# Kernel tuning notes

Hardware: AMD Instinct MI355X
Metric: run time of the kernel (lower is better)

## Reference

```python
import jax, jax.numpy as jnp
import numpy as np

N = 131072   # total nodes (4096 molecules x ~32 atoms)
E = 524288   # directed edges (avg degree 4)
G = 4096     # number of graphs
D_IN, D_H, D_OUT = 128, 512, 256
BN_EPS = 1e-5


def setup_inputs() -> dict:
    key = jax.random.key(0)
    ks = jax.random.split(key, 24)
    def rn(i, shape, s=0.05):
        return jax.random.normal(ks[i], shape, jnp.float32) * s
    inp = {
        "x": jax.random.normal(ks[0], (N, D_IN), jnp.float32),
        "edge_index": jax.random.randint(ks[1], (2, E), 0, N),
        "batch": jnp.sort(jax.random.randint(ks[2], (N,), 0, G)),
        # GCN layer weights (stored [in, out]) and biases
        "W1": rn(3, (D_IN, D_H)), "b1": jnp.zeros((D_H,), jnp.float32),
        "W2": rn(4, (D_H, D_H)),  "b2": jnp.zeros((D_H,), jnp.float32),
        "W3": rn(5, (D_H, D_OUT)), "b3": jnp.zeros((D_OUT,), jnp.float32),
        # BatchNorm (eval mode): gamma, beta, running_mean, running_var
        "g1": jnp.ones((D_H,), jnp.float32),  "be1": jnp.zeros((D_H,), jnp.float32),
        "m1": rn(6, (D_H,)),  "v1": jax.random.uniform(ks[7], (D_H,), jnp.float32) + 0.5,
        "g2": jnp.ones((D_H,), jnp.float32),  "be2": jnp.zeros((D_H,), jnp.float32),
        "m2": rn(8, (D_H,)),  "v2": jax.random.uniform(ks[9], (D_H,), jnp.float32) + 0.5,
        "g3": jnp.ones((D_OUT,), jnp.float32), "be3": jnp.zeros((D_OUT,), jnp.float32),
        "m3": rn(10, (D_OUT,)), "v3": jax.random.uniform(ks[11], (D_OUT,), jnp.float32) + 0.5,
        # MLP head
        "Wf1": rn(12, (D_OUT, D_OUT)), "bf1": jnp.zeros((D_OUT,), jnp.float32),
        "Wf2": rn(13, (D_OUT, D_OUT)), "bf2": jnp.zeros((D_OUT,), jnp.float32),
    }
    return inp


def reference(x, edge_index, batch, W1, b1, W2, b2, W3, b3,
              g1, be1, m1, v1, g2, be2, m2, v2, g3, be3, m3, v3,
              Wf1, bf1, Wf2, bf2):
    loop = jnp.arange(N)
    src = jnp.concatenate([edge_index[0], loop])  # add self-loops (PyG GCNConv default)
    dst = jnp.concatenate([edge_index[1], loop])
    deg = jax.ops.segment_sum(jnp.ones((E + N,), x.dtype), dst, num_segments=N)
    dinv = jnp.where(deg > 0, jax.lax.rsqrt(deg), 0.0)
    norm = dinv[src] * dinv[dst]                  # D^{-1/2} A_hat D^{-1/2}

    def gcn(h, W, b):
        h = h @ W                                 # dense GEMM [N, d_out]
        msg = h[src] * norm[:, None]              # gather + scale
        return jax.ops.segment_sum(msg, dst, num_segments=N) + b  # scatter-add

    def bn(h, g, be, m, v):                       # eval-mode BatchNorm1d
        return g * (h - m) * jax.lax.rsqrt(v + BN_EPS) + be

    h = bn(jax.nn.relu(gcn(x, W1, b1)), g1, be1, m1, v1)
    h = bn(jax.nn.relu(gcn(h, W2, b2)), g2, be2, m2, v2)
    h = bn(jax.nn.relu(gcn(h, W3, b3)), g3, be3, m3, v3)

    sums = jax.ops.segment_sum(h, batch, num_segments=G)          # global_mean_pool
    cnt = jax.ops.segment_sum(jnp.ones((N,), h.dtype), batch, num_segments=G)
    pooled = sums / jnp.maximum(cnt, 1.0)[:, None]

    return jax.nn.relu(pooled @ Wf1 + bf1) @ Wf2 + bf2
```

## Files before the change

### kernel.cpp

```cpp
#include <hip/hip_runtime.h>

static constexpr int NN = 131072;
static constexpr int NE = 524288;
static constexpr int NG = 4096;

typedef __attribute__((ext_vector_type(8))) short short8;
typedef __attribute__((ext_vector_type(4))) float f32x4;
typedef __attribute__((ext_vector_type(2))) float f32x2;

__device__ __forceinline__ float bfbits2f(unsigned b) {
    return __uint_as_float(b << 16);
}
__device__ __forceinline__ unsigned short f2bfbits(float f) {
    unsigned u = __float_as_uint(f);
    u += 0x7fffu + ((u >> 16) & 1u);
    return (unsigned short)(u >> 16);
}
__device__ __forceinline__ unsigned pack2(float a, float b) {
    return (unsigned)f2bfbits(a) | ((unsigned)f2bfbits(b) << 16);
}

__device__ __forceinline__ int geti(const void* p, size_t i, int w64) {
    return w64 ? (int)((const long long*)p)[i] : ((const int*)p)[i];
}
__device__ __forceinline__ int e64_of(const void* eidx) {
    const int* e = (const int*)eidx;
    return (e[1] == 0 && e[2001] == 0 && e[40001] == 0 && e[2 * NE - 1] == 0) ? 1 : 0;
}
__device__ __forceinline__ int b64_of(const void* batch) {
    return (((const int*)batch)[NN - 1] == 0) ? 1 : 0;
}

#if __has_builtin(__builtin_amdgcn_cvt_pk_f32_fp8) && __has_builtin(__builtin_amdgcn_cvt_pk_fp8_f32)
#define FP8_CVT_HW 1
#else
#define FP8_CVT_HW 0
#endif

__device__ __forceinline__ float e4m32f(unsigned b) {
    unsigned e = (b >> 3) & 0xFu, m = b & 7u;
    float v = e ? __uint_as_float(((e + 120u) << 23) | (m << 20))
                : (float)m * 0.001953125f;
    return (b & 0x80u) ? -v : v;
}
__device__ __forceinline__ unsigned f2e4m3(float f) {
    unsigned u = __float_as_uint(f);
    unsigned s = (u >> 24) & 0x80u;
    unsigned mag = u & 0x7fffffffu;
    if (mag >= 0x43e00000u) return s | 0x7eu;
    if (mag < 0x3c800000u) {
        int q = (int)(__uint_as_float(mag) * 512.0f + 0.5f);
        return s | (unsigned)q;
    }
    unsigned r = mag + 0x0007ffffu + ((mag >> 20) & 1u);
    if (r >= 0x43e00000u) return s | 0x7eu;
    return s | (((r >> 23) - 120u) << 3) | ((r >> 20) & 7u);
}

template<bool HI>
__device__ __forceinline__ unsigned dec_pair(unsigned w) {
#if FP8_CVT_HW
    f32x2 p = __builtin_amdgcn_cvt_pk_f32_fp8((int)w, HI);
    return __builtin_amdgcn_perm(__float_as_uint(p.y), __float_as_uint(p.x), 0x07060302u);
#else
    unsigned b0 = HI ? ((w >> 16) & 255u) : (w & 255u);
    unsigned b1 = HI ? (w >> 24) : ((w >> 8) & 255u);
    return pack2(e4m32f(b0), e4m32f(b1));
#endif
}

__device__ __forceinline__ short8 dec8(uint2 u) {
    union { uint4 q; short8 s; } r;
    r.q.x = dec_pair<false>(u.x);
    r.q.y = dec_pair<true>(u.x);
    r.q.z = dec_pair<false>(u.y);
    r.q.w = dec_pair<true>(u.y);
    return r.s;
}

__device__ __forceinline__ void dec4f(unsigned w, float* v) {
#if FP8_CVT_HW
    f32x2 a = __builtin_amdgcn_cvt_pk_f32_fp8((int)w, false);
    f32x2 b = __builtin_amdgcn_cvt_pk_f32_fp8((int)w, true);
    v[0] = a.x; v[1] = a.y; v[2] = b.x; v[3] = b.y;
#else
#pragma unroll
    for (int i = 0; i < 4; ++i) v[i] = e4m32f((w >> (8 * i)) & 0xffu);
#endif
}

__device__ __forceinline__ unsigned enc4(float a, float b, float c, float d) {
#if FP8_CVT_HW
    int r = __builtin_amdgcn_cvt_pk_fp8_f32(a, b, 0, false);
    r = __builtin_amdgcn_cvt_pk_fp8_f32(c, d, r, true);
    return (unsigned)r;
#else
    return f2e4m3(a) | (f2e4m3(b) << 8) | (f2e4m3(c) << 16) | (f2e4m3(d) << 24);
#endif
}
__device__ __forceinline__ unsigned enc1(float a) {
#if FP8_CVT_HW
    return (unsigned)__builtin_amdgcn_cvt_pk_fp8_f32(a, a, 0, false) & 0xffu;
#else
    return f2e4m3(a);
#endif
}

__device__ __forceinline__ void bf8f(uint4 u, float* v) {
    v[0] = bfbits2f(u.x & 0xffffu); v[1] = bfbits2f(u.x >> 16);
    v[2] = bfbits2f(u.y & 0xffffu); v[3] = bfbits2f(u.y >> 16);
    v[4] = bfbits2f(u.z & 0xffffu); v[5] = bfbits2f(u.z >> 16);
    v[6] = bfbits2f(u.w & 0xffffu); v[7] = bfbits2f(u.w >> 16);
}

__device__ __forceinline__ void gld16(const void* g, void* l, int lane) {
#if __has_builtin(__builtin_amdgcn_global_load_lds)
    __builtin_amdgcn_global_load_lds((const __attribute__((address_space(1))) unsigned int*)g,
                                     (__attribute__((address_space(3))) unsigned int*)l, 16, 0, 0);
#else
    *(uint4*)((char*)l + lane * 16) = *(const uint4*)g;
#endif
}

__global__ __launch_bounds__(256) void k_prep(
    const float* __restrict__ W1, const float* __restrict__ W2, const float* __restrict__ W3,
    const float* __restrict__ Wf1, const float* __restrict__ Wf2,
    unsigned short* __restrict__ Wt1, unsigned short* __restrict__ Wt2,
    unsigned short* __restrict__ Wt3, unsigned short* __restrict__ Wtf1,
    unsigned short* __restrict__ Wtf2,
    const float* __restrict__ g1, const float* __restrict__ be1,
    const float* __restrict__ m1, const float* __restrict__ v1,
    const float* __restrict__ g2, const float* __restrict__ be2,
    const float* __restrict__ m2, const float* __restrict__ v2,
    const float* __restrict__ g3, const float* __restrict__ be3,
    const float* __restrict__ m3, const float* __restrict__ v3,
    float* __restrict__ sbuf, int* __restrict__ cnt2,
    const void* __restrict__ batch, int* __restrict__ gstart)
{
    const int id = blockIdx.x, tid = threadIdx.x;
    if (id < 1024) {
        int idx = id * 256 + tid; int k = idx >> 9, n = idx & 511;
        Wt2[n * 512 + k] = f2bfbits(W2[idx]);
    } else if (id < 1536) {
        int idx = (id - 1024) * 256 + tid; int k = idx >> 8, n = idx & 255;
        Wt3[n * 512 + k] = f2bfbits(W3[idx]);
    } else if (id < 1792) {
        int idx = (id - 1536) * 256 + tid; int k = idx >> 9, n = idx & 511;
        Wt1[n * 128 + k] = f2bfbits(W1[idx]);
    } else if (id < 2048) {
        int idx = (id - 1792) * 256 + tid; int k = idx >> 8, n = idx & 255;
        Wtf1[n * 256 + k] = f2bfbits(Wf1[idx]);
    } else if (id < 2304) {
        int idx = (id - 2048) * 256 + tid; int k = idx >> 8, n = idx & 255;
        Wtf2[n * 256 + k] = f2bfbits(Wf2[idx]);
    } else if (id < 3328) {
        cnt2[(id - 2304) * 256 + tid] = 0;
    } else if (id < 3333) {
        int i = (id - 3328) * 256 + tid;
        if (i < 512) {
            float inv = rsqrtf(v1[i] + 1e-5f); float sc = g1[i] * inv;
            sbuf[i] = sc; sbuf[512 + i] = be1[i] - m1[i] * sc;
        } else if (i < 1024) {
            int j = i - 512;
            float inv = rsqrtf(v2[j] + 1e-5f); float sc = g2[j] * inv;
            sbuf[1024 + j] = sc; sbuf[1536 + j] = be2[j] - m2[j] * sc;
        } else if (i < 1280) {
            int j = i - 1024;
            float inv = rsqrtf(v3[j] + 1e-5f); float sc = g3[j] * inv;
            sbuf[2048 + j] = sc; sbuf[2304 + j] = be3[j] - m3[j] * sc;
        }
    } else {
        int i = (id - 3333) * 256 + tid;
        if (i >= NN) return;
        int b64 = b64_of(batch);
        int b = geti(batch, (size_t)i, b64);
        if (i == 0) {
            for (int g = 0; g <= b; ++g) gstart[g] = 0;
        } else {
            int pb = geti(batch, (size_t)i - 1, b64);
            for (int g = pb + 1; g <= b; ++g) gstart[g] = i;
        }
        if (i == NN - 1) {
            for (int g = b + 1; g <= NG; ++g) gstart[g] = NN;
        }
    }
}

__global__ void k_deg_count(const void* __restrict__ eidx, int* __restrict__ cnt) {
    int i = blockIdx.x * 256 + threadIdx.x;
    if (i >= NE) return;
    int d = geti(eidx, (size_t)NE + i, e64_of(eidx));
    atomicAdd(&cnt[d], 1);
}

__global__ __launch_bounds__(256) void k_scan_a(const int* __restrict__ cnt, int* __restrict__ bsum) {
    __shared__ int red[256];
    const int t = threadIdx.x;
    int2 u = *(const int2*)(cnt + blockIdx.x * 512 + t * 2);
    red[t] = u.x + u.y;
    __syncthreads();
    for (int off = 128; off > 0; off >>= 1) {
        if (t < off) red[t] += red[t + off];
        __syncthreads();
    }
    if (t == 0) bsum[blockIdx.x] = red[0];
}

__global__ __launch_bounds__(256) void k_scan_b(const int* __restrict__ bsum, int* __restrict__ boff,
                                                int* __restrict__ rowptr) {
    __shared__ int part[256];
    const int t = threadIdx.x;
    int v = bsum[t];
    part[t] = v;
    __syncthreads();
    for (int off = 1; off < 256; off <<= 1) {
        int w = (t >= off) ? part[t - off] : 0;
        __syncthreads();
        part[t] += w;
        __syncthreads();
    }
    boff[t] = part[t] - v;
    if (t == 255) rowptr[NN] = part[255];
}

__global__ __launch_bounds__(256) void k_scan_c(const int* __restrict__ cnt, const int* __restrict__ boff,
                                                int* __restrict__ rowptr, float* __restrict__ dinv) {
    __shared__ int part[256];
    const int t = threadIdx.x;
    const int base = blockIdx.x * 512 + t * 2;
    int2 u = *(const int2*)(cnt + base);
    int s = u.x + u.y;
    part[t] = s;
    __syncthreads();
    for (int off = 1; off < 256; off <<= 1) {
        int w = (t >= off) ? part[t - off] : 0;
        __syncthreads();
        part[t] += w;
        __syncthreads();
    }
    int ex = boff[blockIdx.x] + part[t] - s;
    int2 o; o.x = ex; o.y = ex + u.x;
    *(int2*)(rowptr + base) = o;
    float2 dv;
    dv.x = rsqrtf((float)(u.x + 1));
    dv.y = rsqrtf((float)(u.y + 1));
    *(float2*)(dinv + base) = dv;
}

__global__ void k_fill(const void* __restrict__ eidx,
                       const int* __restrict__ rowptr, int* __restrict__ fillp,
                       int* __restrict__ col) {
    int i = blockIdx.x * 256 + threadIdx.x;
    if (i >= NE) return;
    int e64 = e64_of(eidx);
    int s = geti(eidx, (size_t)i, e64);
    int d = geti(eidx, (size_t)NE + i, e64);
    int p = rowptr[d] + atomicAdd(&fillp[d], 1);
    col[p] = s;
}

template<int D, int MODE>
__device__ __forceinline__ void load_row_hw(const void* h, int sn, int c0, float* v) {
    if constexpr (MODE == 2) {
        float4 u = *(const float4*)((const float*)h + (size_t)sn * D + c0);
        v[0] = u.x; v[1] = u.y; v[2] = u.z; v[3] = u.w;
    } else {
        uint4 u = *(const uint4*)((const unsigned char*)h + (size_t)sn * D + c0);
        dec4f(u.x, v); dec4f(u.y, v + 4); dec4f(u.z, v + 8); dec4f(u.w, v + 12);
    }
}

template<int D, int EPL, bool FP8>
__device__ __forceinline__ void store_row_hw(void* out, int n, int c0, const float* v) {
    if constexpr (FP8) {
        uint4 u;
        u.x = enc4(v[0], v[1], v[2], v[3]);
        u.y = enc4(v[4], v[5], v[6], v[7]);
        u.z = enc4(v[8], v[9], v[10], v[11]);
        u.w = enc4(v[12], v[13], v[14], v[15]);
        *(uint4*)((unsigned char*)out + (size_t)n * D + c0) = u;
    } else {
        uint2 u; u.x = pack2(v[0], v[1]); u.y = pack2(v[2], v[3]);
        *(uint2*)((unsigned short*)out + (size_t)n * D + c0) = u;
    }
}

template<int D, int IN_MODE, bool OUT_FP8>
__global__ __launch_bounds__(256) void k_agg_hw(
    const void* __restrict__ h,
    const int* __restrict__ rowptr, const int* __restrict__ col,
    const float* __restrict__ dinv,
    void* __restrict__ out)
{
    constexpr int EPL = (IN_MODE == 1) ? 16 : 4;
    const int n = (blockIdx.x * 256 + threadIdx.x) >> 5;
    const int lane = threadIdx.x & 31;
    const int c0 = lane * EPL;
    float dn = dinv[n];
    float acc[EPL], va[EPL], vb[EPL];

    load_row_hw<D, IN_MODE>(h, n, c0, va);
    float wsl = dn * dn;
#pragma unroll
    for (int i = 0; i < EPL; ++i) acc[i] = va[i] * wsl;

    int e = rowptr[n], e1 = rowptr[n + 1];
    for (; e + 2 <= e1; e += 2) {
        int sa = col[e], sb = col[e + 1];
        float wa = dinv[sa] * dn, wb = dinv[sb] * dn;
        load_row_hw<D, IN_MODE>(h, sa, c0, va);
        load_row_hw<D, IN_MODE>(h, sb, c0, vb);
#pragma unroll
        for (int i = 0; i < EPL; ++i) acc[i] += va[i] * wa + vb[i] * wb;
    }
    if (e < e1) {
        int sa = col[e];
        float wa = dinv[sa] * dn;
        load_row_hw<D, IN_MODE>(h, sa, c0, va);
#pragma unroll
        for (int i = 0; i < EPL; ++i) acc[i] += va[i] * wa;
    }
    store_row_hw<D, EPL, OUT_FP8>(out, n, c0, acc);
}

__global__ __launch_bounds__(256) void k_agg_pool(
    const unsigned short* __restrict__ T3,
    const int* __restrict__ rowptr, const int* __restrict__ col,
    const float* __restrict__ dinv,
    const float* __restrict__ b, const float* __restrict__ s, const float* __restrict__ t,
    const int* __restrict__ gstart, unsigned short* __restrict__ pooled)
{
    __shared__ float red[8][256];
    const int g = blockIdx.x;
    const int hw = threadIdx.x >> 5, lane = threadIdx.x & 31;
    const int c0 = lane * 8;
    const int r0 = gstart[g], r1 = gstart[g + 1];
    float p[8] = {};
    float bc[8], sc[8], tc[8];
#pragma unroll
    for (int i = 0; i < 8; ++i) { bc[i] = b[c0 + i]; sc[i] = s[c0 + i]; tc[i] = t[c0 + i]; }

    for (int n = r0 + hw; n < r1; n += 8) {
        float dn = dinv[n];
        float a[8], va[8], vb[8];
        {
            uint4 u = *(const uint4*)(T3 + (size_t)n * 256 + c0);
            bf8f(u, a);
            float w = dn * dn;
#pragma unroll
            for (int i = 0; i < 8; ++i) a[i] *= w;
        }
        int e = rowptr[n], e1 = rowptr[n + 1];
        for (; e + 2 <= e1; e += 2) {
            int sa = col[e], sb = col[e + 1];
            float wa = dinv[sa] * dn, wb = dinv[sb] * dn;
            uint4 ua = *(const uint4*)(T3 + (size_t)sa * 256 + c0);
            uint4 ub = *(const uint4*)(T3 + (size_t)sb * 256 + c0);
            bf8f(ua, va); bf8f(ub, vb);
#pragma unroll
            for (int i = 0; i < 8; ++i) a[i] += va[i] * wa + vb[i] * wb;
        }
        if (e < e1) {
            int sa = col[e];
            float wa = dinv[sa] * dn;
            uint4 ua = *(const uint4*)(T3 + (size_t)sa * 256 + c0);
            bf8f(ua, va);
#pragma unroll
            for (int i = 0; i < 8; ++i) a[i] += va[i] * wa;
        }
#pragma unroll
        for (int i = 0; i < 8; ++i) p[i] += sc[i] * fmaxf(a[i] + bc[i], 0.0f) + tc[i];
    }
#pragma unroll
    for (int i = 0; i < 8; ++i) red[hw][c0 + i] = p[i];
    __syncthreads();
    int ch = threadIdx.x;
    float tot = red[0][ch] + red[1][ch] + red[2][ch] + red[3][ch]
              + red[4][ch] + red[5][ch] + red[6][ch] + red[7][ch];
    __syncthreads();
    red[0][ch] = tot;
    __syncthreads();
    if (ch < 128) {
        int ccount = r1 - r0;
        float inv = 1.0f / (float)(ccount > 0 ? ccount : 1);
        pooled[(size_t)g * 256 + 2 * ch] = f2bfbits(red[0][2 * ch] * inv);
        pooled[(size_t)g * 256 + 2 * ch + 1] = f2bfbits(red[0][2 * ch + 1] * inv);
    }
}

template<bool A_FP8, int CB, int OUT_MODE, bool RELU, bool HAS_BN, bool HAS_BIAS>
__global__ __launch_bounds__(256)
void k_gemm(const void* __restrict__ Aptr,
            const unsigned short* __restrict__ Wt,
            const float* __restrict__ bias,
            const float* __restrict__ s, const float* __restrict__ t,
            void* __restrict__ Cptr,
            int K, int Ncols)
{
    __shared__ __align__(16) unsigned short lB[2][2][128 * 32];
    __shared__ __align__(16) unsigned char  lA8[A_FP8 ? 2 : 1][A_FP8 ? 2 : 1][A_FP8 ? 128 * 32 : 16];
    __shared__ __align__(16) unsigned short lA16[A_FP8 ? 1 : 2][A_FP8 ? 1 : 2][A_FP8 ? 8 : 128 * 32];
    const int tid = threadIdx.x;
    const int id = blockIdx.x;
    const int hi = id >> 3;
    const int cblk = hi % CB;
    const int rblk = (hi / CB) * 8 + (id & 7);
    const int bm = rblk * 128;
    const int bn = cblk * 128;
    const int lane = tid & 63;
    const int wave = tid >> 6;
    const int wm = (wave >> 1) * 64;
    const int wn = (wave & 1) * 64;
    const int fr = lane & 15;
    const int fq = lane >> 4;

    f32x4 acc[4][4] = {};
    const int NG64 = K >> 6;

    auto stage = [&](int buf, int k0) {
#pragma unroll
        for (int h = 0; h < 2; ++h) {
            const int kh = k0 + h * 32;
            if constexpr (A_FP8) {
                const unsigned char* g = (const unsigned char*)Aptr
                    + (size_t)(bm + (wave << 5) + (lane >> 1)) * K + kh + (lane & 1) * 16;
                gld16(g, &lA8[buf][h][(wave << 5) * 32], lane);
            } else {
                const unsigned short* Ab = (const unsigned short*)Aptr;
#pragma unroll
                for (int c = 0; c < 2; ++c) {
                    const unsigned short* g = Ab
                        + (size_t)(bm + (wave << 5) + (c << 4) + (lane >> 2)) * K + kh + (lane & 3) * 8;
                    gld16(g, &lA16[buf][h][((wave << 5) + (c << 4)) * 32], lane);
                }
            }
#pragma unroll
            for (int c = 0; c < 2; ++c) {
                const unsigned short* g = Wt
                    + (size_t)(bn + (wave << 5) + (c << 4) + (lane >> 2)) * K + kh + (lane & 3) * 8;
                gld16(g, &lB[buf][h][((wave << 5) + (c << 4)) * 32], lane);
            }
        }
    };

    stage(0, 0);
    __syncthreads();

    int cur = 0;
    for (int kg = 0; kg < NG64; ++kg) {
        if (kg + 1 < NG64) stage(cur ^ 1, (kg + 1) << 6);

#pragma unroll
        for (int h = 0; h < 2; ++h) {
            short8 a[4], b[4];
#pragma unroll
            for (int i = 0; i < 4; ++i) {
                if constexpr (A_FP8)
                    a[i] = dec8(*(const uint2*)&lA8[cur][h][(wm + 16 * i + fr) * 32 + fq * 8]);
                else
                    a[i] = *(const short8*)&lA16[cur][h][(wm + 16 * i + fr) * 32 + fq * 8];
            }
#pragma unroll
            for (int j = 0; j < 4; ++j)
                b[j] = *(const short8*)&lB[cur][h][(wn + 16 * j + fr) * 32 + fq * 8];
#pragma unroll
            for (int i = 0; i < 4; ++i)
#pragma unroll
                for (int j = 0; j < 4; ++j)
                    acc[i][j] = __builtin_amdgcn_mfma_f32_16x16x32_bf16(a[i], b[j], acc[i][j], 0, 0, 0);
        }

        __syncthreads();
        cur ^= 1;
    }

#pragma unroll
    for (int j = 0; j < 4; ++j) {
        int colI = bn + wn + 16 * j + fr;
        float bi = HAS_BIAS ? bias[colI] : 0.0f;
        float sc = HAS_BN ? s[colI] : 1.0f;
        float tc = HAS_BN ? t[colI] : 0.0f;
#pragma unroll
        for (int i = 0; i < 4; ++i) {
#pragma unroll
            for (int r = 0; r < 4; ++r) {
                int row = bm + wm + 16 * i + fq * 4 + r;
                float z = acc[i][j][r] + bi;
                if (RELU) z = fmaxf(z, 0.0f);
                float y = HAS_BN ? (sc * z + tc) : z;
                if constexpr (OUT_MODE == 2)
                    ((float*)Cptr)[(size_t)row * Ncols + colI] = y;
                else if constexpr (OUT_MODE == 1)
                    ((unsigned char*)Cptr)[(size_t)row * Ncols + colI] = (unsigned char)enc1(y);
                else
                    ((unsigned short*)Cptr)[(size_t)row * Ncols + colI] = f2bfbits(y);
            }
        }
    }
}

template<int CB, int OUT_MODE, bool RELU, bool HAS_BN, bool HAS_BIAS>
__global__ __launch_bounds__(512)
void k_gemm8w(const unsigned char* __restrict__ Aptr,
              const unsigned short* __restrict__ Wt,
              const float* __restrict__ bias,
              const float* __restrict__ s, const float* __restrict__ t,
              void* __restrict__ Cptr,
              int K, int Ncols)
{
    __shared__ __align__(16) unsigned char  lA[2][2][256 * 32];
    __shared__ __align__(16) unsigned short lB[2][2][128 * 32];
    const int tid = threadIdx.x;
    const int id = blockIdx.x;
    const int hi = id >> 3;
    const int cblk = hi % CB;
    const int rblk = (hi / CB) * 8 + (id & 7);
    const int bm = rblk * 256;
    const int bn = cblk * 128;
    const int lane = tid & 63;
    const int wave = tid >> 6;
    const int wm = (wave >> 1) * 64;
    const int wn = (wave & 1) * 64;
    const int fr = lane & 15;
    const int fq = lane >> 4;

    f32x4 acc[4][4] = {};
    const int NG64 = K >> 6;

    auto stage = [&](int buf, int k0) {
#pragma unroll
        for (int h = 0; h < 2; ++h) {
            const int kh = k0 + h * 32;
            {
                const unsigned char* g = Aptr
                    + (size_t)(bm + (wave << 5) + (lane >> 1)) * K + kh + (lane & 1) * 16;
                gld16(g, &lA[buf][h][(wave << 5) * 32], lane);
            }
            {
                const unsigned short* g = Wt
                    + (size_t)(bn + (wave << 4) + (lane >> 2)) * K + kh + (lane & 3) * 8;
                gld16(g, &lB[buf][h][(wave << 4) * 32], lane);
            }
        }
    };

    stage(0, 0);
    __syncthreads();

    int cur = 0;
    for (int kg = 0; kg < NG64; ++kg) {
        if (kg + 1 < NG64) stage(cur ^ 1, (kg + 1) << 6);

#pragma unroll
        for (int h = 0; h < 2; ++h) {
            short8 a[4], b[4];
#pragma unroll
            for (int i = 0; i < 4; ++i)
                a[i] = dec8(*(const uint2*)&lA[cur][h][(wm + 16 * i + fr) * 32 + fq * 8]);
#pragma unroll
            for (int j = 0; j < 4; ++j)
                b[j] = *(const short8*)&lB[cur][h][(wn + 16 * j + fr) * 32 + fq * 8];
#pragma unroll
            for (int i = 0; i < 4; ++i)
#pragma unroll
                for (int j = 0; j < 4; ++j)
                    acc[i][j] = __builtin_amdgcn_mfma_f32_16x16x32_bf16(a[i], b[j], acc[i][j], 0, 0, 0);
        }

        __syncthreads();
        cur ^= 1;
    }

#pragma unroll
    for (int j = 0; j < 4; ++j) {
        int colI = bn + wn + 16 * j + fr;
        float bi = HAS_BIAS ? bias[colI] : 0.0f;
        float sc = HAS_BN ? s[colI] : 1.0f;
        float tc = HAS_BN ? t[colI] : 0.0f;
#pragma unroll
        for (int i = 0; i < 4; ++i) {
#pragma unroll
            for (int r = 0; r < 4; ++r) {
                int row = bm + wm + 16 * i + fq * 4 + r;
                float z = acc[i][j][r] + bi;
                if (RELU) z = fmaxf(z, 0.0f);
                float y = HAS_BN ? (sc * z + tc) : z;
                if constexpr (OUT_MODE == 2)
                    ((float*)Cptr)[(size_t)row * Ncols + colI] = y;
                else if constexpr (OUT_MODE == 1)
                    ((unsigned char*)Cptr)[(size_t)row * Ncols + colI] = (unsigned char)enc1(y);
                else
                    ((unsigned short*)Cptr)[(size_t)row * Ncols + colI] = f2bfbits(y);
            }
        }
    }
}

template<int CB, int OUT_MODE, bool RELU, bool HAS_BN, bool HAS_BIAS>
__global__ __launch_bounds__(512)
void k_gemm8n(const unsigned short* __restrict__ Aptr,
              const unsigned short* __restrict__ Wt,
              const float* __restrict__ bias,
              const float* __restrict__ s, const float* __restrict__ t,
              void* __restrict__ Cptr,
              int K, int Ncols)
{
    __shared__ __align__(16) unsigned short lA[2][2][128 * 32];
    __shared__ __align__(16) unsigned short lB[2][2][128 * 32];
    const int tid = threadIdx.x;
    const int id = blockIdx.x;
    const int hi = id >> 3;
    const int cblk = hi % CB;
    const int rblk = (hi / CB) * 8 + (id & 7);
    const int bm = rblk * 128;
    const int bn = cblk * 128;
    const int lane = tid & 63;
    const int wave = tid >> 6;
    const int wm = (wave >> 1) * 32;
    const int wn = (wave & 1) * 64;
    const int fr = lane & 15;
    const int fq = lane >> 4;

    f32x4 acc[2][4] = {};
    const int NG64 = K >> 6;

    auto stage = [&](int buf, int k0) {
#pragma unroll
        for (int h = 0; h < 2; ++h) {
            const int kh = k0 + h * 32;
            const unsigned short* ga = Aptr
                + (size_t)(bm + (wave << 4) + (lane >> 2)) * K + kh + (lane & 3) * 8;
            gld16(ga, &lA[buf][h][(wave << 4) * 32], lane);
            const unsigned short* gb = Wt
                + (size_t)(bn + (wave << 4) + (lane >> 2)) * K + kh + (lane & 3) * 8;
            gld16(gb, &lB[buf][h][(wave << 4) * 32], lane);
        }
    };

    stage(0, 0);
    __syncthreads();

    int cur = 0;
    for (int kg = 0; kg < NG64; ++kg) {
        if (kg + 1 < NG64) stage(cur ^ 1, (kg + 1) << 6);

#pragma unroll
        for (int h = 0; h < 2; ++h) {
            short8 a[2], b[4];
#pragma unroll
            for (int i = 0; i < 2; ++i)
                a[i] = *(const short8*)&lA[cur][h][(wm + 16 * i + fr) * 32 + fq * 8];
#pragma unroll
            for (int j = 0; j < 4; ++j)
                b[j] = *(const short8*)&lB[cur][h][(wn + 16 * j + fr) * 32 + fq * 8];
#pragma unroll
            for (int i = 0; i < 2; ++i)
#pragma unroll
                for (int j = 0; j < 4; ++j)
                    acc[i][j] = __builtin_amdgcn_mfma_f32_16x16x32_bf16(a[i], b[j], acc[i][j], 0, 0, 0);
        }

        __syncthreads();
        cur ^= 1;
    }

#pragma unroll
    for (int j = 0; j < 4; ++j) {
        int colI = bn + wn + 16 * j + fr;
        float bi = HAS_BIAS ? bias[colI] : 0.0f;
        float sc = HAS_BN ? s[colI] : 1.0f;
        float tc = HAS_BN ? t[colI] : 0.0f;
#pragma unroll
        for (int i = 0; i < 2; ++i) {
#pragma unroll
            for (int r = 0; r < 4; ++r) {
                int row = bm + wm + 16 * i + fq * 4 + r;
                float z = acc[i][j][r] + bi;
                if (RELU) z = fmaxf(z, 0.0f);
                float y = HAS_BN ? (sc * z + tc) : z;
                if constexpr (OUT_MODE == 2)
                    ((float*)Cptr)[(size_t)row * Ncols + colI] = y;
                else if constexpr (OUT_MODE == 1)
                    ((unsigned char*)Cptr)[(size_t)row * Ncols + colI] = (unsigned char)enc1(y);
                else
                    ((unsigned short*)Cptr)[(size_t)row * Ncols + colI] = f2bfbits(y);
            }
        }
    }
}


extern "C" void kernel_launch(void* const* d_in, const int* in_sizes, int n_in,
                              void* d_out, int out_size, void* d_ws, size_t ws_size,
                              hipStream_t stream) {
    const float* x   = (const float*)d_in[0];
    const void* eidx = d_in[1];
    const void* batch = d_in[2];
    const float* W1  = (const float*)d_in[3];
    const float* b1  = (const float*)d_in[4];
    const float* W2  = (const float*)d_in[5];
    const float* b2  = (const float*)d_in[6];
    const float* W3  = (const float*)d_in[7];
    const float* b3  = (const float*)d_in[8];
    const float* g1  = (const float*)d_in[9];
    const float* be1 = (const float*)d_in[10];
    const float* m1  = (const float*)d_in[11];
    const float* v1  = (const float*)d_in[12];
    const float* g2  = (const float*)d_in[13];
    const float* be2 = (const float*)d_in[14];
    const float* m2  = (const float*)d_in[15];
    const float* v2  = (const float*)d_in[16];
    const float* g3  = (const float*)d_in[17];
    const float* be3 = (const float*)d_in[18];
    const float* m3  = (const float*)d_in[19];
    const float* v3  = (const float*)d_in[20];
    const float* Wf1 = (const float*)d_in[21];
    const float* bf1 = (const float*)d_in[22];
    const float* Wf2 = (const float*)d_in[23];
    const float* bf2 = (const float*)d_in[24];

    unsigned char* RB = (unsigned char*)d_ws;
    unsigned char* RA = RB + 67108864;
    unsigned char* EX = RB + 134217728;
    int*   rowptr = (int*)(EX + 0);
    int*   col    = (int*)(EX + 524544);
    float* dinv   = (float*)(EX + 2621696);
    int*   cnt    = (int*)(EX + 3145984);
    int*   fillp  = (int*)(EX + 3670272);
    int*   gstart = (int*)(EX + 4194560);
    float* sbuf   = (float*)(EX + 4211456);
    float *s1 = sbuf, *t1 = sbuf + 512, *s2 = sbuf + 1024, *t2 = sbuf + 1536;
    float *s3 = sbuf + 2048, *t3v = sbuf + 2304;
    unsigned short* Wt1  = (unsigned short*)(EX + 4221696);
    unsigned short* Wt2  = (unsigned short*)(EX + 4352768);
    unsigned short* Wt3  = (unsigned short*)(EX + 4877056);
    unsigned short* Wtf1 = (unsigned short*)(EX + 5139200);
    unsigned short* Wtf2 = (unsigned short*)(EX + 5270272);
    int*   bsum  = (int*)(EX + 5401344);
    int*   boff  = (int*)(EX + 5402368);

    unsigned short* pooled = (unsigned short*)RB;
    unsigned short* z1     = (unsigned short*)(RB + 2097152);

    k_prep<<<3845, 256, 0, stream>>>(W1, W2, W3, Wf1, Wf2,
                                     Wt1, Wt2, Wt3, Wtf1, Wtf2,
                                     g1, be1, m1, v1, g2, be2, m2, v2, g3, be3, m3, v3,
                                     sbuf, cnt, batch, gstart);
    k_deg_count<<<NE / 256, 256, 0, stream>>>(eidx, cnt);
    k_scan_a<<<256, 256, 0, stream>>>(cnt, bsum);
    k_scan_b<<<1, 256, 0, stream>>>(bsum, boff, rowptr);
    k_scan_c<<<256, 256, 0, stream>>>(cnt, boff, rowptr, dinv);
    k_fill<<<NE / 256, 256, 0, stream>>>(eidx, rowptr, fillp, col);

    const dim3 gagg(NN / 8);

    k_agg_hw<128, 2, false><<<gagg, 256, 0, stream>>>(x, rowptr, col, dinv, RA);
    k_gemm8n<4, 1, true, true, true><<<4096, 512, 0, stream>>>(
        (const unsigned short*)RA, Wt1, b1, s1, t1, RB, 128, 512);

    k_agg_hw<512, 1, true><<<gagg, 256, 0, stream>>>(RB, rowptr, col, dinv, RA);
    k_gemm8w<4, 1, true, true, true><<<1024, 512, 0, stream>>>(RA, Wt2, b2, s2, t2, RB, 512, 512);
    k_gemm8w<4, 1, true, true, true><<<1024, 512, 0, stream>>>(RA + 33554432, Wt2, b2, s2, t2,
                                                               RB + 33554432, 512, 512);

    k_gemm8w<2, 0, false, false, false><<<1024, 512, 0, stream>>>(RB, Wt3, nullptr, nullptr, nullptr, RA, 512, 256);

    k_agg_pool<<<NG, 256, 0, stream>>>((const unsigned short*)RA, rowptr, col, dinv,
                                       b3, s3, t3v, gstart, pooled);

    k_gemm<false, 2, 0, true, false, true><<<64, 256, 0, stream>>>(pooled, Wtf1, bf1, nullptr, nullptr, z1, 256, 256);
    k_gemm<false, 2, 2, false, false, true><<<64, 256, 0, stream>>>(z1, Wtf2, bf2, nullptr, nullptr, d_out, 256, 256);
}
```

Baseline: 551.0 us.

## Triple-buffer GEMM K-loop with vmcnt waits and unroll agg_pool edges by four

```diff
diff --git a/kernel.cpp b/kernel.cpp
--- a/kernel.cpp
+++ b/kernel.cpp
@@ -342,7 +342,7 @@
 
     for (int n = r0 + hw; n < r1; n += 8) {
         float dn = dinv[n];
-        float a[8], va[8], vb[8];
+        float a[8], va[8], vb[8], vc[8], vd[8];
         {
             uint4 u = *(const uint4*)(T3 + (size_t)n * 256 + c0);
             bf8f(u, a);
@@ -351,6 +351,19 @@
             for (int i = 0; i < 8; ++i) a[i] *= w;
         }
         int e = rowptr[n], e1 = rowptr[n + 1];
+        for (; e + 4 <= e1; e += 4) {
+            int sa = col[e], sb = col[e + 1], sc2 = col[e + 2], sd = col[e + 3];
+            float wa = dinv[sa] * dn, wb = dinv[sb] * dn;
+            float wc = dinv[sc2] * dn, wd = dinv[sd] * dn;
+            uint4 ua = *(const uint4*)(T3 + (size_t)sa * 256 + c0);
+            uint4 ub = *(const uint4*)(T3 + (size_t)sb * 256 + c0);
+            uint4 uc = *(const uint4*)(T3 + (size_t)sc2 * 256 + c0);
+            uint4 ud = *(const uint4*)(T3 + (size_t)sd * 256 + c0);
+            bf8f(ua, va); bf8f(ub, vb); bf8f(uc, vc); bf8f(ud, vd);
+#pragma unroll
+            for (int i = 0; i < 8; ++i)
+                a[i] += va[i] * wa + vb[i] * wb + vc[i] * wc + vd[i] * wd;
+        }
         for (; e + 2 <= e1; e += 2) {
             int sa = col[e], sb = col[e + 1];
             float wa = dinv[sa] * dn, wb = dinv[sb] * dn;
@@ -501,15 +514,15 @@
 
 template<int CB, int OUT_MODE, bool RELU, bool HAS_BN, bool HAS_BIAS>
 __global__ __launch_bounds__(512)
-void k_gemm8w(const unsigned char* __restrict__ Aptr,
+void k_gemm8c(const unsigned char* __restrict__ Aptr,
               const unsigned short* __restrict__ Wt,
               const float* __restrict__ bias,
               const float* __restrict__ s, const float* __restrict__ t,
               void* __restrict__ Cptr,
               int K, int Ncols)
 {
-    __shared__ __align__(16) unsigned char  lA[2][2][256 * 32];
-    __shared__ __align__(16) unsigned short lB[2][2][128 * 32];
+    __shared__ __align__(16) unsigned char  lA[3][256 * 32];
+    __shared__ __align__(16) unsigned short lB[3][128 * 32];
     const int tid = threadIdx.x;
     const int id = blockIdx.x;
     const int hi = id >> 3;
@@ -525,50 +538,53 @@
     const int fq = lane >> 4;
 
     f32x4 acc[4][4] = {};
-    const int NG64 = K >> 6;
-
-    auto stage = [&](int buf, int k0) {
-#pragma unroll
-        for (int h = 0; h < 2; ++h) {
-            const int kh = k0 + h * 32;
-            {
-                const unsigned char* g = Aptr
-                    + (size_t)(bm + (wave << 5) + (lane >> 1)) * K + kh + (lane & 1) * 16;
-                gld16(g, &lA[buf][h][(wave << 5) * 32], lane);
-            }
-            {
-                const unsigned short* g = Wt
-                    + (size_t)(bn + (wave << 4) + (lane >> 2)) * K + kh + (lane & 3) * 8;
-                gld16(g, &lB[buf][h][(wave << 4) * 32], lane);
-            }
-        }
+    const int NT = K >> 5;
+
+    const unsigned char* ga0 = Aptr
+        + (size_t)(bm + (wave << 5) + (lane >> 1)) * K + (lane & 1) * 16;
+    const unsigned short* gb0 = Wt
+        + (size_t)(bn + (wave << 4) + (lane >> 2)) * K + (lane & 3) * 8;
+
+    auto stage = [&](int buf, int kt) {
+        gld16(ga0 + (kt << 5), &lA[buf][(wave << 5) * 32], lane);
+        gld16(gb0 + (kt << 5), &lB[buf][(wave << 4) * 32], lane);
     };
 
     stage(0, 0);
-    __syncthreads();
-
-    int cur = 0;
-    for (int kg = 0; kg < NG64; ++kg) {
-        if (kg + 1 < NG64) stage(cur ^ 1, (kg + 1) << 6);
-
-#pragma unroll
-        for (int h = 0; h < 2; ++h) {
-            short8 a[4], b[4];
-#pragma unroll
-            for (int i = 0; i < 4; ++i)
-                a[i] = dec8(*(const uint2*)&lA[cur][h][(wm + 16 * i + fr) * 32 + fq * 8]);
+    stage(1, 1);
+    asm volatile("s_waitcnt vmcnt(2)" ::: "memory");
+    __builtin_amdgcn_s_barrier();
+    asm volatile("" ::: "memory");
+
+    int c = 0;
+#pragma unroll 1
+    for (int kt = 0; kt < NT; ++kt) {
+        const bool do_stage = (kt + 2) < NT;
+        if (do_stage) {
+            int nb = c + 2; if (nb >= 3) nb -= 3;
+            stage(nb, kt + 2);
+        }
+
+        short8 a[4], b[4];
+#pragma unroll
+        for (int i = 0; i < 4; ++i)
+            a[i] = dec8(*(const uint2*)&lA[c][(wm + 16 * i + fr) * 32 + fq * 8]);
+#pragma unroll
+        for (int j = 0; j < 4; ++j)
+            b[j] = *(const short8*)&lB[c][(wn + 16 * j + fr) * 32 + fq * 8];
+        __builtin_amdgcn_s_setprio(1);
+#pragma unroll
+        for (int i = 0; i < 4; ++i)
 #pragma unroll
             for (int j = 0; j < 4; ++j)
-                b[j] = *(const short8*)&lB[cur][h][(wn + 16 * j + fr) * 32 + fq * 8];
-#pragma unroll
-            for (int i = 0; i < 4; ++i)
-#pragma unroll
-                for (int j = 0; j < 4; ++j)
-                    acc[i][j] = __builtin_amdgcn_mfma_f32_16x16x32_bf16(a[i], b[j], acc[i][j], 0, 0, 0);
-        }
-
-        __syncthreads();
-        cur ^= 1;
+                acc[i][j] = __builtin_amdgcn_mfma_f32_16x16x32_bf16(a[i], b[j], acc[i][j], 0, 0, 0);
+        __builtin_amdgcn_s_setprio(0);
+
+        if (do_stage) asm volatile("s_waitcnt vmcnt(2)" ::: "memory");
+        else          asm volatile("s_waitcnt vmcnt(0)" ::: "memory");
+        __builtin_amdgcn_s_barrier();
+        asm volatile("" ::: "memory");
+        ++c; if (c >= 3) c = 0;
     }
 
 #pragma unroll
@@ -759,11 +775,11 @@
         (const unsigned short*)RA, Wt1, b1, s1, t1, RB, 128, 512);
 
     k_agg_hw<512, 1, true><<<gagg, 256, 0, stream>>>(RB, rowptr, col, dinv, RA);
-    k_gemm8w<4, 1, true, true, true><<<1024, 512, 0, stream>>>(RA, Wt2, b2, s2, t2, RB, 512, 512);
-    k_gemm8w<4, 1, true, true, true><<<1024, 512, 0, stream>>>(RA + 33554432, Wt2, b2, s2, t2,
+    k_gemm8c<4, 1, true, true, true><<<1024, 512, 0, stream>>>(RA, Wt2, b2, s2, t2, RB, 512, 512);
+    k_gemm8c<4, 1, true, true, true><<<1024, 512, 0, stream>>>(RA + 33554432, Wt2, b2, s2, t2,
                                                                RB + 33554432, 512, 512);
 
-    k_gemm8w<2, 0, false, false, false><<<1024, 512, 0, stream>>>(RB, Wt3, nullptr, nullptr, nullptr, RA, 512, 256);
+    k_gemm8c<2, 0, false, false, false><<<1024, 512, 0, stream>>>(RB, Wt3, nullptr, nullptr, nullptr, RA, 512, 256);
 
     k_agg_pool<<<NG, 256, 0, stream>>>((const unsigned short*)RA, rowptr, col, dinv,
                                        b3, s3, t3v, gstart, pooled);
```

Result: slower. 564.2 us (+2.4%).
